# Optimization experiments

Measured on AMD Instinct MI355X. Metric: run time of the kernel, lower is better.

## Reference

```python
import jax, jax.numpy as jnp
import numpy as np

P = 8        # patch_size
S = 4        # stride
NV = 31      # nvals
DELTA = 0.05
ETA = 0.01
TAU = 0.1
H = W = 256
C = 3
HP = (H - P) // S + 1
WP = (W - P) // S + 1

_lin = jnp.linspace(-1.0, 1.0, P)
# torch.meshgrid 'ij': meshy varies along rows, meshx along cols; shape (1,P,P,1,1)
YG = jnp.broadcast_to(_lin[:, None], (P, P))[None, :, :, None, None]
XG = jnp.broadcast_to(_lin[None, :], (P, P))[None, :, :, None, None]


def unfold(x):
    # x: (b,c,H,W) -> (b,c,P,P,hp,wp)
    i = (jnp.arange(HP) * S)[:, None] + jnp.arange(P)[None, :]  # (hp,P)
    j = (jnp.arange(WP) * S)[:, None] + jnp.arange(P)[None, :]  # (wp,P)
    pat = x[:, :, i[:, None, :, None], j[None, :, None, :]]    # (b,c,hp,wp,P,P)
    return jnp.transpose(pat, (0, 1, 4, 5, 2, 3))


def fold(patches):
    # patches: (b,c,P,P,hp,wp) -> (b,c,H,W) via overlap-add
    b, c = patches.shape[:2]
    i = (jnp.arange(HP) * S)[:, None] + jnp.arange(P)[None, :]  # (hp,P)
    j = (jnp.arange(WP) * S)[:, None] + jnp.arange(P)[None, :]
    ii = jnp.broadcast_to(i.T[:, None, :, None], (P, P, HP, WP))
    jj = jnp.broadcast_to(j.T[None, :, None, :], (P, P, HP, WP))
    out = jnp.zeros((b, c, H, W), patches.dtype)
    return out.at[:, :, ii, jj].add(patches)


def params_to_distances(params):
    # params: (N,5,hp,wp) -> distances (N,2,P,P,hp,wp)
    x0 = params[:, 3][:, None, None]  # (N,1,1,hp,wp)
    y0 = params[:, 4][:, None, None]
    angles = jnp.sort(jnp.remainder(params[:, :3], 2 * jnp.pi), axis=1)
    a1 = angles[:, 0][:, None, None]
    a2 = angles[:, 1][:, None, None]
    a3 = angles[:, 2][:, None, None]
    a4 = 0.5 * (a1 + a3) + jnp.where(
        jnp.remainder(0.5 * (a1 - a3), 2 * jnp.pi) >= jnp.pi, jnp.pi, 0.0)

    def g(dt):
        return (dt / jnp.pi - 1.0) ** 35

    def hline(a):
        return -jnp.sin(a) * (XG - x0) + jnp.cos(a) * (YG - y0)

    r42 = jnp.remainder(a2 - a4, 2 * jnp.pi)
    sgn42 = jnp.where(r42 < jnp.pi, 1.0, -1.0)
    d42 = sgn42 * jnp.minimum(sgn42 * hline(a4), -sgn42 * hline(a2)) + g(r42) * TAU

    r13 = jnp.remainder(a3 - a1, 2 * jnp.pi)
    sgn13 = jnp.where(r13 < jnp.pi, 1.0, -1.0)
    d13 = sgn13 * jnp.minimum(sgn13 * hline(a1), -sgn13 * hline(a3)) + g(r13) * TAU
    return jnp.stack([d13, d42], axis=1)


def distances_to_indicators(dists):
    # dists: (N,2,P,P,hp,wp) -> wedges (N,3,P,P,hp,wp)
    h = 0.5 * (1.0 + (2.0 / jnp.pi) * jnp.arctan(dists / ETA))
    return jnp.stack([1.0 - h[:, 0], h[:, 0] * (1.0 - h[:, 1]), h[:, 0] * h[:, 1]], axis=1)


def distances_to_boundaries(dists):
    d1 = dists[:, 0:1]
    d2 = dists[:, 1:2]
    minabs = jnp.where(d1 < 0.0, -d1,
                       jnp.where(d2 < 0.0, jnp.minimum(d1, -d2), jnp.minimum(d1, d2)))
    return 1.0 / (1.0 + (minabs / DELTA) ** 2)


def colors_and_patches(wedges, img_pat):
    # wedges: (N,3,P,P,hp,wp); img_pat: (1,c,P,P,hp,wp)
    num = jnp.einsum('cijhw,nkijhw->nckhw', img_pat[0], wedges)
    den = wedges.sum(axis=(2, 3))  # (N,3,hp,wp)
    colors = num / (den[:, None] + 1e-10)  # (N,c,3,hp,wp)
    patches = jnp.einsum('nkijhw,nckhw->ncijhw', wedges, colors)
    return colors, patches


def setup_inputs() -> dict:
    key = jax.random.key(0)
    x = jax.random.uniform(key, (1, C, H, W), dtype=jnp.float32)
    return {"x": x}


def reference(x):
    img_pat = unfold(x)  # (1,c,P,P,hp,wp)
    num_patches = fold(jnp.ones((1, 1, P, P, HP, WP), x.dtype))[0, 0]  # (H,W)

    angle_range = jnp.linspace(0.0, 2 * np.pi, NV + 1)[:NV]
    xy_range = jnp.linspace(-3.0, 3.0, NV)

    params = jnp.zeros((1, 5, HP, WP), x.dtype)
    # Coordinate-descent grid search over the 5 junction parameters
    for i in range(5):
        rng = angle_range if i < 3 else xy_range
        pq = jnp.tile(params, (NV, 1, 1, 1))
        pq = pq.at[:, i].add(rng[:, None, None])
        dists = params_to_distances(pq)
        wedges = distances_to_indicators(dists)
        _, patches = colors_and_patches(wedges, img_pat)
        loss = ((img_pat - patches) ** 2).mean(axis=(1, 2, 3))  # (NV,hp,wp)
        best = jnp.argmin(loss, axis=0)                          # (hp,wp)
        params = params.at[0, i].set(params[0, i] + rng[best])

    dists = params_to_distances(params)
    wedges = distances_to_indicators(dists)
    _, patches = colors_and_patches(wedges, img_pat)
    global_image = fold(patches) / num_patches
    local_boundaries = distances_to_boundaries(dists)  # (1,1,P,P,hp,wp)
    global_boundaries = fold(local_boundaries) / num_patches
    return global_image, global_boundaries
```

## Files before the change

### kernel.cpp

```cpp
#include <hip/hip_runtime.h>
#include <math.h>

#define WP_ 63
#define NPATCH 3969
#define PI_D 3.141592653589793
#define TWO_PI_D 6.283185307179586476925287
#define BANDF 4e-3f

typedef float f32x2 __attribute__((ext_vector_type(2)));
__device__ __forceinline__ f32x2 v2(float s) { return (f32x2){s, s}; }
__device__ __forceinline__ f32x2 fma2(f32x2 a, f32x2 b, f32x2 c) {
  return __builtin_elementwise_fma(a, b, c);
}

__device__ __forceinline__ double remtp_d(double v) {
  double r = (v < 0.0) ? v + TWO_PI_D : v;
  r = (r < 0.0) ? r + TWO_PI_D : r;
  r = (r >= TWO_PI_D) ? r - TWO_PI_D : r;
  return r;
}

__device__ __forceinline__ double lin8d(int i) {
  if (i == 7) return 1.0;
  return __dadd_rn(__dmul_rn((double)i, 2.0 / 7.0), -1.0);
}
__device__ __forceinline__ double angd(int n) {
  return __dmul_rn((double)n, TWO_PI_D / 31.0);
}
__device__ __forceinline__ double xyd(int n) {
  if (n == 30) return 3.0;
  return __dadd_rn(__dmul_rn((double)n, 6.0 / 30.0), -3.0);
}

__device__ __forceinline__ double pow35_d(double x) {
#pragma clang fp contract(off)
  double x2 = x * x;
  double r = x * x2;
  double b = x2 * x2;
  b = b * b; b = b * b; b = b * b;
  return r * b;
}

__device__ __forceinline__ double rcp_nr(double d) {
  double r;
  asm("v_rcp_f64 %0, %1" : "=v"(r) : "v"(d));
  r = fma(fma(-d, r, 1.0), r, r);
  r = fma(fma(-d, r, 1.0), r, r);
  return r;
}

__device__ __forceinline__ void sincos_fast(double x, double* so, double* co) {
  double kd = rint(x * 6.36619772367581382433e-01);
  int q = (int)kd & 3;
  double r = fma(-kd, 1.57079632673412561417e+00, x);
  r = fma(-kd, 6.07710050650619224932e-11, r);
  double z = r * r;
  double ps = 1.58969099521155010221e-10;
  ps = fma(z, ps, -2.50507602534068634195e-08);
  ps = fma(z, ps, 2.75573137070700676789e-06);
  ps = fma(z, ps, -1.98412698298579493134e-04);
  ps = fma(z, ps, 8.33333333332248946124e-03);
  ps = fma(z, ps, -1.66666666666666324348e-01);
  double sr = fma(z * r, ps, r);
  double pc = -1.13596475577881948265e-11;
  pc = fma(z, pc, 2.08757232129817482790e-09);
  pc = fma(z, pc, -2.75573143513906633035e-07);
  pc = fma(z, pc, 2.48015872894767294178e-05);
  pc = fma(z, pc, -1.38888888888741095749e-03);
  pc = fma(z, pc, 4.16666666666666019037e-02);
  double cr = fma(z, fma(z, pc, -0.5), 1.0);
  bool swp = q & 1;
  double s0 = swp ? cr : sr;
  double c0 = swp ? sr : cr;
  *so = (q & 2) ? -s0 : s0;
  *co = (((q + 1) & 2)) ? -c0 : c0;
}

#define TABN 57
__device__ __forceinline__ void build_atan_tab(double2* tab, float2* tabf) {
  int k = threadIdx.x;
  if (k < 56) {
    int hi = ((4076 + k) << 18) | (1 << 17);
    double c = __hiloint2double(hi, 0);
    double a = atan(c);
    tab[k] = double2{c, a};
    tabf[k + 1] = float2{(float)c, (float)a};
  } else if (k == 56) {
    tab[56] = double2{0.0, 0.0};
    tabf[0] = float2{0.0f, 0.0f};
  }
}

__device__ __forceinline__ void hstep2_tab(const double2* __restrict__ tab,
                                           double da, double db,
                                           double& ha, double& hb) {
  double za = da * 100.0, zb = db * 100.0;
  double ua = fabs(za), ub = fabs(zb);
  int ia = (__double2hiint(ua) >> 18) - 4076;
  int ib = (__double2hiint(ub) >> 18) - 4076;
  ia = (ia < 0) ? 56 : ((ia > 55) ? 55 : ia);
  ib = (ib < 0) ? 56 : ((ib > 55) ? 55 : ib);
  double2 ea = tab[ia];
  double2 eb = tab[ib];
  double ta = (ua - ea.x) * rcp_nr(fma(ua, ea.x, 1.0));
  double tb = (ub - eb.x) * rcp_nr(fma(ub, eb.x, 1.0));
  double z2a = ta * ta, z2b = tb * tb;
  double pa = 1.0 / 13.0, pb = 1.0 / 13.0;
  pa = fma(z2a, pa, -1.0 / 11.0); pb = fma(z2b, pb, -1.0 / 11.0);
  pa = fma(z2a, pa, 1.0 / 9.0);   pb = fma(z2b, pb, 1.0 / 9.0);
  pa = fma(z2a, pa, -1.0 / 7.0);  pb = fma(z2b, pb, -1.0 / 7.0);
  pa = fma(z2a, pa, 1.0 / 5.0);   pb = fma(z2b, pb, 1.0 / 5.0);
  pa = fma(z2a, pa, -1.0 / 3.0);  pb = fma(z2b, pb, -1.0 / 3.0);
  pa = fma(z2a, pa, 1.0);         pb = fma(z2b, pb, 1.0);
  double aa = fma(ta, pa, ea.y);
  double ab = fma(tb, pb, eb.y);
  aa = copysign(aa, za);
  ab = copysign(ab, zb);
  ha = fma(aa, 0.31830988618379067154, 0.5);
  hb = fma(ab, 0.31830988618379067154, 0.5);
}

__device__ __forceinline__ f32x2 hstepv(const float2* __restrict__ tabf,
                                        f32x2 d) {
  f32x2 z = d * 100.0f;
  f32x2 u = __builtin_elementwise_abs(z);
  int ia = (int)(__float_as_uint(u.x) >> 21) - 492;
  int ib = (int)(__float_as_uint(u.y) >> 21) - 492;
  ia = min(max(ia, -1), 55) + 1;
  ib = min(max(ib, -1), 55) + 1;
  float2 ea = tabf[ia], eb = tabf[ib];
  f32x2 ec = {ea.x, eb.x};
  f32x2 ey = {ea.y, eb.y};
  f32x2 den = fma2(u, ec, v2(1.0f));
  float ra, rb;
  asm("v_rcp_f32 %0, %1" : "=v"(ra) : "v"(den.x));
  asm("v_rcp_f32 %0, %1" : "=v"(rb) : "v"(den.y));
  f32x2 r = {ra, rb};
  f32x2 t = (u - ec) * r;
  f32x2 p = fma2(t * t, v2(-0.33333334f), v2(1.0f));
  f32x2 a = fma2(t, p, ey);
  a = __builtin_elementwise_copysign(a, z);
  return fma2(a, v2(0.31830987f), v2(0.5f));
}

struct JPd {
  double s1, c1, s2, c2, s3, c3, s4, c4;
  double sg13, sg42, gt13, gt42;
};

__device__ JPd jprep_d(double p0, double p1, double p2) {
#pragma clang fp contract(off)
  double r0 = remtp_d(p0), r1 = remtp_d(p1), r2 = remtp_d(p2);
  double mn = fmin(r0, r1), mx = fmax(r0, r1);
  double a1 = fmin(mn, r2);
  double a3 = fmax(mx, r2);
  double a2 = fmax(mn, fmin(mx, r2));
  double remm = remtp_d(0.5 * (a1 - a3));
  double a4 = 0.5 * (a1 + a3) + ((remm >= PI_D) ? PI_D : 0.0);
  JPd j;
  double r42 = remtp_d(a2 - a4);
  j.sg42 = (r42 < PI_D) ? 1.0 : -1.0;
  j.gt42 = pow35_d(r42 / PI_D - 1.0) * 0.1;
  double r13 = remtp_d(a3 - a1);
  j.sg13 = (r13 < PI_D) ? 1.0 : -1.0;
  j.gt13 = pow35_d(r13 / PI_D - 1.0) * 0.1;
  sincos_fast(a1, &j.s1, &j.c1);
  sincos_fast(a2, &j.s2, &j.c2);
  sincos_fast(a3, &j.s3, &j.c3);
  sincos_fast(a4, &j.s4, &j.c4);
  return j;
}

__device__ __forceinline__ void jdist_d(const JPd& j, double dx, double dy,
                                        double& d13, double& d42) {
  double hl1 = (-j.s1) * dx + j.c1 * dy;
  double hl2 = (-j.s2) * dx + j.c2 * dy;
  double hl3 = (-j.s3) * dx + j.c3 * dy;
  double hl4 = (-j.s4) * dx + j.c4 * dy;
  d13 = j.sg13 * fmin(j.sg13 * hl1, (-j.sg13) * hl3) + j.gt13;
  d42 = j.sg42 * fmin(j.sg42 * hl4, (-j.sg42) * hl2) + j.gt42;
}

__global__ void __launch_bounds__(256)
foj_descent(const float* __restrict__ x, double* __restrict__ pout) {
  const int tid = threadIdx.x;
  const int wv = tid >> 6;
  const int lane = tid & 63;
  const int hp = lane >> 5;
  const int cand = lane & 31;
  const int patch = blockIdx.x * 4 + wv;

  __shared__ double2 stab[TABN];
  __shared__ float2 stabf[TABN + 1];
  __shared__ float4 simg[4][64];
  __shared__ float simgp[4][3][64];
  build_atan_tab(stab, stabf);
  if (patch < NPATCH) {
    int ph = patch / WP_;
    int pw = patch - ph * WP_;
    int py = lane >> 3, pxx = lane & 7;
    int base = (ph * 4 + py) * 256 + (pw * 4 + pxx);
    float4 v;
    v.x = x[base];
    v.y = x[65536 + base];
    v.z = x[131072 + base];
    v.w = 0.0f;
    simg[wv][lane] = v;
    simgp[wv][0][lane] = v.x;
    simgp[wv][1][lane] = v.y;
    simgp[wv][2][lane] = v.z;
  }
  __syncthreads();
  if (patch >= NPATCH) return;
  const float4* sp = simg[wv];

  double sx0 = 0.0, sx1 = 0.0, sx2 = 0.0;
  {
    const float4* hbase = sp + hp * 32;
#pragma unroll
    for (int t = 0; t < 32; ++t) {
      float4 im = hbase[t];
      sx0 += (double)im.x; sx1 += (double)im.y; sx2 += (double)im.z;
    }
    sx0 += __shfl_xor(sx0, 32);
    sx1 += __shfl_xor(sx1, 32);
    sx2 += __shfl_xor(sx2, 32);
  }
  const float sx0f = (float)sx0, sx1f = (float)sx1, sx2f = (float)sx2;

  double q0 = 0.0, q1 = 0.0, q2 = 0.0, q3 = 0.0, q4 = 0.0;

#pragma unroll 1
  for (int i = 0; i < 5; ++i) {
    double rv = (i < 3) ? angd(cand) : xyd(cand);
    double p0 = q0 + ((i == 0) ? rv : 0.0);
    double p1 = q1 + ((i == 1) ? rv : 0.0);
    double p2 = q2 + ((i == 2) ? rv : 0.0);
    double x0 = q3 + ((i == 3) ? rv : 0.0);
    double y0 = q4 + ((i == 4) ? rv : 0.0);

    JPd j = jprep_d(p0, p1, p2);

    float blf;
    {
      f32x2 ns1v = v2((float)(-j.s1)), ns2v = v2((float)(-j.s2));
      f32x2 ns3v = v2((float)(-j.s3)), ns4v = v2((float)(-j.s4));
      float c1f = (float)j.c1, c2f = (float)j.c2;
      float c3f = (float)j.c3, c4f = (float)j.c4;
      f32x2 sg13v = v2((float)j.sg13), sg42v = v2((float)j.sg42);
      f32x2 nsg13v = -sg13v, nsg42v = -sg42v;
      f32x2 gt13v = v2((float)j.gt13), gt42v = v2((float)j.gt42);
      f32x2 dxp[4];
#pragma unroll
      for (int t = 0; t < 4; ++t)
        dxp[t] = (f32x2){(float)(lin8d(2 * t) - x0),
                         (float)(lin8d(2 * t + 1) - x0)};

      f32x2 den0v = {0, 0}, den1v = {0, 0}, den2v = {0, 0};
      f32x2 n00v = {0, 0}, n01v = {0, 0}, n10v = {0, 0}, n11v = {0, 0};
      f32x2 n20v = {0, 0}, n21v = {0, 0};
      f32x2 W00v = {0, 0}, W01v = {0, 0}, W11v = {0, 0};
#pragma unroll 1
      for (int r = 0; r < 4; ++r) {
        int iyy = hp * 4 + r;
        double liny = (iyy == 7) ? 1.0
                    : __dadd_rn(__dmul_rn((double)iyy, 2.0 / 7.0), -1.0);
        float dyf = (float)(liny - y0);
        f32x2 cdy1 = v2(c1f * dyf), cdy2 = v2(c2f * dyf);
        f32x2 cdy3 = v2(c3f * dyf), cdy4 = v2(c4f * dyf);
        const float* q0p = &simgp[wv][0][hp * 32 + r * 8];
        const float* q1p = &simgp[wv][1][hp * 32 + r * 8];
        const float* q2p = &simgp[wv][2][hp * 32 + r * 8];
#pragma unroll
        for (int cp = 0; cp < 4; ++cp) {
          f32x2 dxv = dxp[cp];
          f32x2 hl1 = fma2(ns1v, dxv, cdy1);
          f32x2 hl3 = fma2(ns3v, dxv, cdy3);
          f32x2 hl4 = fma2(ns4v, dxv, cdy4);
          f32x2 hl2 = fma2(ns2v, dxv, cdy2);
          f32x2 d13 = fma2(sg13v,
              __builtin_elementwise_min(sg13v * hl1, nsg13v * hl3), gt13v);
          f32x2 d42 = fma2(sg42v,
              __builtin_elementwise_min(sg42v * hl4, nsg42v * hl2), gt42v);
          f32x2 h1 = hstepv(stabf, d13);
          f32x2 h2 = hstepv(stabf, d42);
          f32x2 w0 = v2(1.0f) - h1;
          f32x2 om = v2(1.0f) - h2;
          f32x2 w1 = h1 * om;
          f32x2 w2 = h1 * h2;
          f32x2 i0 = *(const f32x2*)(q0p + 2 * cp);
          f32x2 i1 = *(const f32x2*)(q1p + 2 * cp);
          f32x2 i2 = *(const f32x2*)(q2p + 2 * cp);
          den0v += w0; den1v += w1; den2v += w2;
          n00v = fma2(i0, w0, n00v); n01v = fma2(i0, w1, n01v);
          n10v = fma2(i1, w0, n10v); n11v = fma2(i1, w1, n11v);
          n20v = fma2(i2, w0, n20v); n21v = fma2(i2, w1, n21v);
          W00v = fma2(w0, w0, W00v); W01v = fma2(w0, w1, W01v);
          W11v = fma2(w1, w1, W11v);
        }
      }
      float den0f = den0v.x + den0v.y, den1f = den1v.x + den1v.y;
      float den2f = den2v.x + den2v.y;
      float n00f = n00v.x + n00v.y, n01f = n01v.x + n01v.y;
      float n10f = n10v.x + n10v.y, n11f = n11v.x + n11v.y;
      float n20f = n20v.x + n20v.y, n21f = n21v.x + n21v.y;
      float W00f = W00v.x + W00v.y, W01f = W01v.x + W01v.y;
      float W11f = W11v.x + W11v.y;

      den0f += __shfl_xor(den0f, 32); den1f += __shfl_xor(den1f, 32); den2f += __shfl_xor(den2f, 32);
      n00f += __shfl_xor(n00f, 32); n01f += __shfl_xor(n01f, 32);
      n10f += __shfl_xor(n10f, 32); n11f += __shfl_xor(n11f, 32);
      n20f += __shfl_xor(n20f, 32); n21f += __shfl_xor(n21f, 32);
      W00f += __shfl_xor(W00f, 32); W01f += __shfl_xor(W01f, 32); W11f += __shfl_xor(W11f, 32);

      float n02f = sx0f - n00f - n01f;
      float n12f = sx1f - n10f - n11f;
      float n22f = sx2f - n20f - n21f;
      float W02f = den0f - W00f - W01f;
      float W12f = den1f - W01f - W11f;
      float W22f = den2f - W02f - W12f;

      float e0 = den0f + 1e-10f, e1 = den1f + 1e-10f, e2 = den2f + 1e-10f;
      float r0f, r1f, r2f;
      asm("v_rcp_f32 %0, %1" : "=v"(r0f) : "v"(e0));
      asm("v_rcp_f32 %0, %1" : "=v"(r1f) : "v"(e1));
      asm("v_rcp_f32 %0, %1" : "=v"(r2f) : "v"(e2));
      r0f = fmaf(fmaf(-e0, r0f, 1.0f), r0f, r0f);
      r1f = fmaf(fmaf(-e1, r1f, 1.0f), r1f, r1f);
      r2f = fmaf(fmaf(-e2, r2f, 1.0f), r2f, r2f);
      float c00 = n00f * r0f, c01 = n01f * r1f, c02 = n02f * r2f;
      float c10 = n10f * r0f, c11 = n11f * r1f, c12 = n12f * r2f;
      float c20 = n20f * r0f, c21 = n21f * r1f, c22 = n22f * r2f;

      float lossf =
          c00 * (W00f * c00 + W01f * c01 + W02f * c02 - 2.0f * n00f) +
          c01 * (W01f * c00 + W11f * c01 + W12f * c02 - 2.0f * n01f) +
          c02 * (W02f * c00 + W12f * c01 + W22f * c02 - 2.0f * n02f) +
          c10 * (W00f * c10 + W01f * c11 + W02f * c12 - 2.0f * n10f) +
          c11 * (W01f * c10 + W11f * c11 + W12f * c12 - 2.0f * n11f) +
          c12 * (W02f * c10 + W12f * c11 + W22f * c12 - 2.0f * n12f) +
          c20 * (W00f * c20 + W01f * c21 + W02f * c22 - 2.0f * n20f) +
          c21 * (W01f * c20 + W11f * c21 + W12f * c22 - 2.0f * n21f) +
          c22 * (W02f * c20 + W12f * c21 + W22f * c22 - 2.0f * n22f);

      blf = (cand < 31) ? lossf : 3.0e38f;
    }

    float mnf = blf;
#pragma unroll
    for (int m = 1; m <= 16; m <<= 1) mnf = fminf(mnf, __shfl_xor(mnf, m));
    bool inb = (cand < 31) && (blf <= mnf + BANDF);
    unsigned bal32 = (unsigned)__ballot(inb);

    int bi;
    if (__popc(bal32) == 1) {
      bi = __ffs(bal32) - 1;
    } else {
      double den0 = 0, den1 = 0, den2 = 0;
      double n00 = 0, n01 = 0, n10 = 0, n11 = 0, n20 = 0, n21 = 0;
      double W00 = 0, W01 = 0, W11 = 0;
#pragma unroll 1
      for (int r = 0; r < 4; ++r) {
        int iyy = hp * 4 + r;
        double liny = (iyy == 7) ? 1.0
                    : __dadd_rn(__dmul_rn((double)iyy, 2.0 / 7.0), -1.0);
        double dy = liny - y0;
        const float4* rowp = sp + hp * 32 + r * 8;
#pragma unroll
        for (int c = 0; c < 8; ++c) {
          double dx = lin8d(c) - x0;
          double d13, d42;
          jdist_d(j, dx, dy, d13, d42);
          double h1, h2;
          hstep2_tab(stab, d13, d42, h1, h2);
          double w0 = 1.0 - h1;
          double w1 = h1 * (1.0 - h2);
          double w2 = h1 * h2;
          float4 im = rowp[c];
          double ix = (double)im.x, iy2 = (double)im.y, iz = (double)im.z;
          den0 += w0; den1 += w1; den2 += w2;
          n00 += ix * w0; n01 += ix * w1;
          n10 += iy2 * w0; n11 += iy2 * w1;
          n20 += iz * w0; n21 += iz * w1;
          W00 += w0 * w0; W01 += w0 * w1; W11 += w1 * w1;
        }
      }
      den0 += __shfl_xor(den0, 32); den1 += __shfl_xor(den1, 32); den2 += __shfl_xor(den2, 32);
      n00 += __shfl_xor(n00, 32); n01 += __shfl_xor(n01, 32);
      n10 += __shfl_xor(n10, 32); n11 += __shfl_xor(n11, 32);
      n20 += __shfl_xor(n20, 32); n21 += __shfl_xor(n21, 32);
      W00 += __shfl_xor(W00, 32); W01 += __shfl_xor(W01, 32); W11 += __shfl_xor(W11, 32);

      double n02 = sx0 - n00 - n01;
      double n12 = sx1 - n10 - n11;
      double n22 = sx2 - n20 - n21;
      double W02 = den0 - W00 - W01;
      double W12 = den1 - W01 - W11;
      double W22 = den2 - W02 - W12;

      double r0 = rcp_nr(den0 + 1e-10);
      double r1 = rcp_nr(den1 + 1e-10);
      double r2 = rcp_nr(den2 + 1e-10);
      double c00 = n00 * r0, c01 = n01 * r1, c02 = n02 * r2;
      double c10 = n10 * r0, c11 = n11 * r1, c12 = n12 * r2;
      double c20 = n20 * r0, c21 = n21 * r1, c22 = n22 * r2;

      double loss =
          c00 * (W00 * c00 + W01 * c01 + W02 * c02 - 2.0 * n00) +
          c01 * (W01 * c00 + W11 * c01 + W12 * c02 - 2.0 * n01) +
          c02 * (W02 * c00 + W12 * c01 + W22 * c02 - 2.0 * n02) +
          c10 * (W00 * c10 + W01 * c11 + W02 * c12 - 2.0 * n10) +
          c11 * (W01 * c10 + W11 * c11 + W12 * c12 - 2.0 * n11) +
          c12 * (W02 * c10 + W12 * c11 + W22 * c12 - 2.0 * n12) +
          c20 * (W00 * c20 + W01 * c21 + W02 * c22 - 2.0 * n20) +
          c21 * (W01 * c20 + W11 * c21 + W12 * c22 - 2.0 * n21) +
          c22 * (W02 * c20 + W12 * c21 + W22 * c22 - 2.0 * n22);

      double bl = (cand < 31) ? loss : (double)INFINITY;
      int bi0 = cand;
#pragma unroll
      for (int m = 1; m <= 16; m <<= 1) {
        double ol = __shfl_xor(bl, m);
        int oi = __shfl_xor(bi0, m);
        if (ol < bl || (ol == bl && oi < bi0)) { bl = ol; bi0 = oi; }
      }
      bi = bi0;
    }

    double upd = (i < 3) ? angd(bi) : xyd(bi);
    if (i == 0) q0 += upd;
    else if (i == 1) q1 += upd;
    else if (i == 2) q2 += upd;
    else if (i == 3) q3 += upd;
    else q4 += upd;
  }

  if (lane == 0) {
    pout[patch * 5 + 0] = q0;
    pout[patch * 5 + 1] = q1;
    pout[patch * 5 + 2] = q2;
    pout[patch * 5 + 3] = q3;
    pout[patch * 5 + 4] = q4;
  }
}

__global__ void __launch_bounds__(256) foj_final(const float* __restrict__ x,
                                                 const double* __restrict__ pin,
                                                 float* __restrict__ out) {
  int lane = threadIdx.x & 63;
  int patch = blockIdx.x * 4 + (threadIdx.x >> 6);
  if (patch >= NPATCH) return;
  int ph = patch / WP_;
  int pw = patch - ph * WP_;
  double q0 = pin[patch * 5 + 0];
  double q1 = pin[patch * 5 + 1];
  double q2 = pin[patch * 5 + 2];
  double x0 = pin[patch * 5 + 3];
  double y0 = pin[patch * 5 + 4];

  JPd j = jprep_d(q0, q1, q2);
  int pi2 = lane >> 3, pj = lane & 7;
  double dx = lin8d(pj) - x0;
  double dy = lin8d(pi2) - y0;
  double d13, d42;
  jdist_d(j, dx, dy, d13, d42);
  double h1 = 0.5 + 0.31830988618379067154 * atan(d13 * 100.0);
  double h2 = 0.5 + 0.31830988618379067154 * atan(d42 * 100.0);
  double w0 = 1.0 - h1;
  double w1 = h1 * (1.0 - h2);
  double w2 = h1 * h2;

  int oy = ph * 4 + pi2, ox = pw * 4 + pj;
  double im0 = (double)x[oy * 256 + ox];
  double im1 = (double)x[65536 + oy * 256 + ox];
  double im2 = (double)x[131072 + oy * 256 + ox];

  double red[12] = {w0, w1, w2,
                    im0 * w0, im0 * w1, im0 * w2,
                    im1 * w0, im1 * w1, im1 * w2,
                    im2 * w0, im2 * w1, im2 * w2};
#pragma unroll
  for (int t = 0; t < 12; ++t) {
    double v = red[t];
#pragma unroll
    for (int m = 1; m <= 32; m <<= 1) v += __shfl_xor(v, m);
    red[t] = v;
  }
  double e0 = red[0] + 1e-10, e1 = red[1] + 1e-10, e2 = red[2] + 1e-10;
  double pv0 = w0 * (red[3] / e0) + w1 * (red[4] / e1) + w2 * (red[5] / e2);
  double pv1 = w0 * (red[6] / e0) + w1 * (red[7] / e1) + w2 * (red[8] / e2);
  double pv2 = w0 * (red[9] / e0) + w1 * (red[10] / e1) + w2 * (red[11] / e2);

  double minabs = (d13 < 0.0) ? -d13
                              : ((d42 < 0.0) ? fmin(d13, -d42) : fmin(d13, d42));
  double tb = minabs / 0.05;
  double bnd = 1.0 / (1.0 + tb * tb);

  atomicAdd(&out[oy * 256 + ox], (float)pv0);
  atomicAdd(&out[65536 + oy * 256 + ox], (float)pv1);
  atomicAdd(&out[131072 + oy * 256 + ox], (float)pv2);
  atomicAdd(&out[196608 + oy * 256 + ox], (float)bnd);
}

__global__ void __launch_bounds__(256) foj_norm(float* __restrict__ out) {
  int idx = blockIdx.x * 256 + threadIdx.x;
  int y = idx >> 8, xx = idx & 255;
  int hlo = (y >= 4) ? ((y - 4) >> 2) : 0;
  int hhi = min(62, y >> 2);
  int wlo = (xx >= 4) ? ((xx - 4) >> 2) : 0;
  int whi = min(62, xx >> 2);
  float np_ = (float)((hhi - hlo + 1) * (whi - wlo + 1));
  out[idx] /= np_;
  out[65536 + idx] /= np_;
  out[131072 + idx] /= np_;
  out[196608 + idx] /= np_;
}

extern "C" void kernel_launch(void* const* d_in, const int* in_sizes, int n_in,
                              void* d_out, int out_size, void* d_ws, size_t ws_size,
                              hipStream_t stream) {
  const float* x = (const float*)d_in[0];
  float* out = (float*)d_out;
  double* pws = (double*)d_ws;

  foj_descent<<<(NPATCH + 3) / 4, 256, 0, stream>>>(x, pws);
  hipMemsetAsync(d_out, 0, (size_t)out_size * sizeof(float), stream);
  foj_final<<<(NPATCH + 3) / 4, 256, 0, stream>>>(x, pws, out);
  foj_norm<<<256, 256, 0, stream>>>(out);
}
```

Measured before the change: 120.3 us.

## Re-evaluate only in-band candidates with one pixel per lane in fallback

The double-precision tie-break fallback used to evaluate all 31 candidates, each lane processing 32 pixels. Now it loops only over the candidates inside the near-tie band. Each candidate's junction parameters are broadcast by shuffle, every lane handles one of the 64 pixels, and the 12 sums are reduced with a full wave butterfly. This avoids spending double-precision work on candidates that cannot win, at the cost of a serial loop per ambiguous candidate and many shuffles.

```diff
diff --git a/kernel.cpp b/kernel.cpp
--- a/kernel.cpp
+++ b/kernel.cpp
@@ -227,6 +227,10 @@
     sx2 += __shfl_xor(sx2, 32);
   }
   const float sx0f = (float)sx0, sx1f = (float)sx1, sx2f = (float)sx2;
+
+  const double vlinx = lin8d(lane & 7);
+  const double vliny = lin8d(lane >> 3);
+  const float4 vim = sp[lane];
 
   double q0 = 0.0, q1 = 0.0, q2 = 0.0, q3 = 0.0, q4 = 0.0;
 
@@ -356,73 +360,76 @@
     if (__popc(bal32) == 1) {
       bi = __ffs(bal32) - 1;
     } else {
-      double den0 = 0, den1 = 0, den2 = 0;
-      double n00 = 0, n01 = 0, n10 = 0, n11 = 0, n20 = 0, n21 = 0;
-      double W00 = 0, W01 = 0, W11 = 0;
+      double bestLoss = (double)INFINITY;
+      int bi0 = 0;
+      unsigned rem = bal32;
 #pragma unroll 1
-      for (int r = 0; r < 4; ++r) {
-        int iyy = hp * 4 + r;
-        double liny = (iyy == 7) ? 1.0
-                    : __dadd_rn(__dmul_rn((double)iyy, 2.0 / 7.0), -1.0);
-        double dy = liny - y0;
-        const float4* rowp = sp + hp * 32 + r * 8;
-#pragma unroll
-        for (int c = 0; c < 8; ++c) {
-          double dx = lin8d(c) - x0;
-          double d13, d42;
-          jdist_d(j, dx, dy, d13, d42);
-          double h1, h2;
-          hstep2_tab(stab, d13, d42, h1, h2);
-          double w0 = 1.0 - h1;
-          double w1 = h1 * (1.0 - h2);
-          double w2 = h1 * h2;
-          float4 im = rowp[c];
-          double ix = (double)im.x, iy2 = (double)im.y, iz = (double)im.z;
-          den0 += w0; den1 += w1; den2 += w2;
-          n00 += ix * w0; n01 += ix * w1;
-          n10 += iy2 * w0; n11 += iy2 * w1;
-          n20 += iz * w0; n21 += iz * w1;
-          W00 += w0 * w0; W01 += w0 * w1; W11 += w1 * w1;
+      while (rem) {
+        int c = __ffs(rem) - 1;
+        rem &= rem - 1;
+        double rvc = (i < 3) ? angd(c) : xyd(c);
+        double x0c = q3 + ((i == 3) ? rvc : 0.0);
+        double y0c = q4 + ((i == 4) ? rvc : 0.0);
+        JPd jc;
+        jc.s1 = __shfl(j.s1, c);  jc.c1 = __shfl(j.c1, c);
+        jc.s2 = __shfl(j.s2, c);  jc.c2 = __shfl(j.c2, c);
+        jc.s3 = __shfl(j.s3, c);  jc.c3 = __shfl(j.c3, c);
+        jc.s4 = __shfl(j.s4, c);  jc.c4 = __shfl(j.c4, c);
+        jc.sg13 = __shfl(j.sg13, c); jc.sg42 = __shfl(j.sg42, c);
+        jc.gt13 = __shfl(j.gt13, c); jc.gt42 = __shfl(j.gt42, c);
+
+        double d13, d42;
+        jdist_d(jc, vlinx - x0c, vliny - y0c, d13, d42);
+        double h1, h2;
+        hstep2_tab(stab, d13, d42, h1, h2);
+        double w0 = 1.0 - h1;
+        double w1 = h1 * (1.0 - h2);
+        double w2 = h1 * h2;
+        double ix = (double)vim.x, iy2 = (double)vim.y, iz = (double)vim.z;
+        double s0 = w0, s1 = w1, s2 = w2;
+        double s3 = ix * w0, s4 = ix * w1;
+        double s5 = iy2 * w0, s6 = iy2 * w1;
+        double s7 = iz * w0, s8 = iz * w1;
+        double s9 = w0 * w0, s10 = w0 * w1, s11 = w1 * w1;
+#pragma unroll
+        for (int m = 1; m <= 32; m <<= 1) {
+          s0 += __shfl_xor(s0, m);  s1 += __shfl_xor(s1, m);
+          s2 += __shfl_xor(s2, m);  s3 += __shfl_xor(s3, m);
+          s4 += __shfl_xor(s4, m);  s5 += __shfl_xor(s5, m);
+          s6 += __shfl_xor(s6, m);  s7 += __shfl_xor(s7, m);
+          s8 += __shfl_xor(s8, m);  s9 += __shfl_xor(s9, m);
+          s10 += __shfl_xor(s10, m); s11 += __shfl_xor(s11, m);
         }
-      }
-      den0 += __shfl_xor(den0, 32); den1 += __shfl_xor(den1, 32); den2 += __shfl_xor(den2, 32);
-      n00 += __shfl_xor(n00, 32); n01 += __shfl_xor(n01, 32);
-      n10 += __shfl_xor(n10, 32); n11 += __shfl_xor(n11, 32);
-      n20 += __shfl_xor(n20, 32); n21 += __shfl_xor(n21, 32);
-      W00 += __shfl_xor(W00, 32); W01 += __shfl_xor(W01, 32); W11 += __shfl_xor(W11, 32);
-
-      double n02 = sx0 - n00 - n01;
-      double n12 = sx1 - n10 - n11;
-      double n22 = sx2 - n20 - n21;
-      double W02 = den0 - W00 - W01;
-      double W12 = den1 - W01 - W11;
-      double W22 = den2 - W02 - W12;
-
-      double r0 = rcp_nr(den0 + 1e-10);
-      double r1 = rcp_nr(den1 + 1e-10);
-      double r2 = rcp_nr(den2 + 1e-10);
-      double c00 = n00 * r0, c01 = n01 * r1, c02 = n02 * r2;
-      double c10 = n10 * r0, c11 = n11 * r1, c12 = n12 * r2;
-      double c20 = n20 * r0, c21 = n21 * r1, c22 = n22 * r2;
-
-      double loss =
-          c00 * (W00 * c00 + W01 * c01 + W02 * c02 - 2.0 * n00) +
-          c01 * (W01 * c00 + W11 * c01 + W12 * c02 - 2.0 * n01) +
-          c02 * (W02 * c00 + W12 * c01 + W22 * c02 - 2.0 * n02) +
-          c10 * (W00 * c10 + W01 * c11 + W02 * c12 - 2.0 * n10) +
-          c11 * (W01 * c10 + W11 * c11 + W12 * c12 - 2.0 * n11) +
-          c12 * (W02 * c10 + W12 * c11 + W22 * c12 - 2.0 * n12) +
-          c20 * (W00 * c20 + W01 * c21 + W02 * c22 - 2.0 * n20) +
-          c21 * (W01 * c20 + W11 * c21 + W12 * c22 - 2.0 * n21) +
-          c22 * (W02 * c20 + W12 * c21 + W22 * c22 - 2.0 * n22);
-
-      double bl = (cand < 31) ? loss : (double)INFINITY;
-      int bi0 = cand;
-#pragma unroll
-      for (int m = 1; m <= 16; m <<= 1) {
-        double ol = __shfl_xor(bl, m);
-        int oi = __shfl_xor(bi0, m);
-        if (ol < bl || (ol == bl && oi < bi0)) { bl = ol; bi0 = oi; }
+        double den0 = s0, den1 = s1, den2 = s2;
+        double n00 = s3, n01 = s4, n10 = s5, n11 = s6, n20 = s7, n21 = s8;
+        double W00 = s9, W01 = s10, W11 = s11;
+
+        double n02 = sx0 - n00 - n01;
+        double n12 = sx1 - n10 - n11;
+        double n22 = sx2 - n20 - n21;
+        double W02 = den0 - W00 - W01;
+        double W12 = den1 - W01 - W11;
+        double W22 = den2 - W02 - W12;
+
+        double r0 = rcp_nr(den0 + 1e-10);
+        double r1 = rcp_nr(den1 + 1e-10);
+        double r2 = rcp_nr(den2 + 1e-10);
+        double c00 = n00 * r0, c01 = n01 * r1, c02 = n02 * r2;
+        double c10 = n10 * r0, c11 = n11 * r1, c12 = n12 * r2;
+        double c20 = n20 * r0, c21 = n21 * r1, c22 = n22 * r2;
+
+        double loss =
+            c00 * (W00 * c00 + W01 * c01 + W02 * c02 - 2.0 * n00) +
+            c01 * (W01 * c00 + W11 * c01 + W12 * c02 - 2.0 * n01) +
+            c02 * (W02 * c00 + W12 * c01 + W22 * c02 - 2.0 * n02) +
+            c10 * (W00 * c10 + W01 * c11 + W02 * c12 - 2.0 * n10) +
+            c11 * (W01 * c10 + W11 * c11 + W12 * c12 - 2.0 * n11) +
+            c12 * (W02 * c10 + W12 * c11 + W22 * c12 - 2.0 * n12) +
+            c20 * (W00 * c20 + W01 * c21 + W02 * c22 - 2.0 * n20) +
+            c21 * (W01 * c20 + W11 * c21 + W12 * c22 - 2.0 * n21) +
+            c22 * (W02 * c20 + W12 * c21 + W22 * c22 - 2.0 * n22);
+
+        if (loss < bestLoss) { bestLoss = loss; bi0 = c; }
       }
       bi = bi0;
     }
```

Measured after the change: 101.5 us. 15.7% less time.
